# Performance work log

Measured on AMD Instinct MI355X. Metric: run time of the kernel, lower is better.

## Reference

```python
import jax, jax.numpy as jnp
import numpy as np

N_ITER = 4  # matches init_kwargs n_iter
N, K, D = 32768, 32, 32


def setup_inputs() -> dict:
    key = jax.random.key(0)
    k1, k2 = jax.random.split(key)
    data = jax.random.normal(k1, (N, D), dtype=jnp.float32)
    # torch init: means ~ randn, covariances = stacked identity, weights uniform
    means = jax.random.normal(k2, (K, D), dtype=jnp.float32)
    covariances = jnp.tile(jnp.eye(D, dtype=jnp.float32)[None], (K, 1, 1))
    weights = jnp.ones((K,), dtype=jnp.float32) / K
    return {"data": data, "means": means, "covariances": covariances, "weights": weights}


def _em(data, means, covariances, weights, n_iter):
    for _ in range(n_iter):
        # ---- E-step (vectorized over components, replacing the python loop) ----
        inv = jnp.linalg.inv(covariances)          # [K,D,D]
        det = jnp.linalg.det(covariances)          # [K]
        diff = data[:, None, :] - means[None]      # [N,K,D]
        # quadratic form diff^T Sigma^{-1} diff per point/component
        q = jnp.einsum('nkd,kde,nke->nk', diff, inv, diff)  # [N,K]
        probs = weights[None, :] * jnp.exp(-0.5 * q) / jnp.sqrt(det)[None, :]
        probs = probs / probs.sum(axis=1, keepdims=True)    # responsibilities [N,K]
        # ---- M-step (torch updates weights first; cov uses diff w.r.t. OLD means) ----
        weights = probs.mean(axis=0)                         # [K]
        Nk = probs.sum(axis=0)                               # [K]
        means = (probs.T @ data) / Nk[:, None]               # [K,D] (new means)
        covariances = jnp.einsum('nk,nkd,nke->kde', probs, diff, diff) / Nk[:, None, None]
    return means, covariances, weights


def reference(data, means, covariances, weights):
    return _em(data, means, covariances, weights, N_ITER)
```

## Files before the change

### kernel.cpp

```cpp
#include <hip/hip_runtime.h>

#define NPTS 32768
#define KK 32
#define DD 32

__global__ __launch_bounds__(256) void init_kernel(
    const float* __restrict__ means0, const float* __restrict__ cov0,
    const float* __restrict__ w0,
    float* __restrict__ meansA, float* __restrict__ covS, float* __restrict__ wS)
{
    int i = blockIdx.x * 256 + threadIdx.x;
    if (i < 1024)  meansA[i] = means0[i];
    if (i < 32768) covS[i]   = cov0[i];
    if (i < 32)    wS[i]     = w0[i];
}

__global__ __launch_bounds__(256) void prep_kernel(
    const float* __restrict__ cov, const float* __restrict__ means_in,
    const float* __restrict__ wts,
    float* __restrict__ A2, float* __restrict__ b2,
    float* __restrict__ cvec, float* __restrict__ coef)
{
    int k   = blockIdx.x;
    int tid = threadIdx.x;
    __shared__ float M[32][66];
    __shared__ float mu[32];
    __shared__ float bb[32];

    for (int i = tid; i < 1024; i += 256) {
        int r = i >> 5, c = i & 31;
        M[r][c]      = cov[k * 1024 + i];
        M[r][32 + c] = (r == c) ? 1.0f : 0.0f;
    }
    if (tid < 32) mu[tid] = means_in[k * 32 + tid];
    __syncthreads();

    int r  = tid >> 3;
    int c0 = (tid & 7) * 8;
    float det = 1.0f;
    for (int s = 0; s < 32; ++s) {
        float piv = M[s][s];
        det *= piv;
        float rp = 1.0f / piv;
        float f  = (r != s) ? M[r][s] : 0.0f;
        __syncthreads();
        if (tid < 64) M[s][tid] *= rp;
        __syncthreads();
        if (r != s) {
            #pragma unroll
            for (int j = 0; j < 8; ++j) M[r][c0 + j] -= f * M[s][c0 + j];
        }
        __syncthreads();
    }

    for (int i = tid; i < 1024; i += 256) {
        int d = i >> 5, e = i & 31;
        float val = M[d][32 + e];
        A2[(i >> 1) * 64 + k * 2 + (i & 1)] = val;
    }
    if (tid < 32) {
        int d = tid;
        float bd = 0.0f;
        #pragma unroll
        for (int e = 0; e < 32; ++e) bd += M[d][32 + e] * mu[e];
        bb[d] = bd;
        b2[(d >> 1) * 64 + k * 2 + (d & 1)] = bd;
    }
    __syncthreads();
    if (tid == 0) {
        float cc = 0.0f;
        #pragma unroll
        for (int d = 0; d < 32; ++d) cc += mu[d] * bb[d];
        cvec[k] = cc;
        coef[k] = wts[k] / sqrtf(det);
    }
}

__global__ __launch_bounds__(1024) void estep_kernel(
    const float* __restrict__ data, const float* __restrict__ A2g,
    const float* __restrict__ b2g, const float* __restrict__ cvec,
    const float* __restrict__ coefg, float* __restrict__ P)
{
    __shared__ alignas(16) float A2s[32768];
    int tid = threadIdx.x;
    for (int i = tid; i < 8192; i += 1024)
        ((float4*)A2s)[i] = ((const float4*)A2g)[i];
    __syncthreads();

    int lane = tid & 63;
    int wv   = tid >> 6;
    int k    = lane & 31;
    int g    = lane >> 5;
    int p0   = blockIdx.x * 64 + wv * 4 + g * 2;

    float x0[32], x1[32];
    const float4* d0p = (const float4*)(data + (size_t)p0 * 32);
    const float4* d1p = (const float4*)(data + (size_t)(p0 + 1) * 32);
    #pragma unroll
    for (int j = 0; j < 8; ++j) {
        float4 v = d0p[j];
        x0[4*j] = v.x; x0[4*j+1] = v.y; x0[4*j+2] = v.z; x0[4*j+3] = v.w;
        float4 u = d1p[j];
        x1[4*j] = u.x; x1[4*j+1] = u.y; x1[4*j+2] = u.z; x1[4*j+3] = u.w;
    }

    float q0 = 0.0f, q1 = 0.0f;
    #pragma unroll
    for (int d = 0; d < 32; ++d) {
        float r0 = 0.0f, s0 = 0.0f, r1 = 0.0f, s1 = 0.0f;
        #pragma unroll
        for (int c = 0; c < 16; ++c) {
            float2 a = *(const float2*)&A2s[(d * 16 + c) * 64 + (k << 1)];
            r0 += a.x * x0[2*c];     s0 += a.y * x0[2*c + 1];
            r1 += a.x * x1[2*c];     s1 += a.y * x1[2*c + 1];
        }
        q0 += x0[d] * (r0 + s0);
        q1 += x1[d] * (r1 + s1);
    }

    float bx0 = 0.0f, bx1 = 0.0f;
    #pragma unroll
    for (int d2 = 0; d2 < 16; ++d2) {
        float2 b = *(const float2*)&b2g[d2 * 64 + (k << 1)];
        bx0 += b.x * x0[2*d2] + b.y * x0[2*d2 + 1];
        bx1 += b.x * x1[2*d2] + b.y * x1[2*d2 + 1];
    }
    float cc = cvec[k], cf = coefg[k];
    float e0 = cf * __expf(-0.5f * (q0 - 2.0f * bx0 + cc));
    float e1 = cf * __expf(-0.5f * (q1 - 2.0f * bx1 + cc));

    float s0r = e0, s1r = e1;
    #pragma unroll
    for (int m = 16; m >= 1; m >>= 1) {
        s0r += __shfl_xor(s0r, m, 64);
        s1r += __shfl_xor(s1r, m, 64);
    }
    P[(size_t)p0 * 32 + k]       = e0 / s0r;
    P[(size_t)(p0 + 1) * 32 + k] = e1 / s1r;
}

#define PSTRIDE 1060
__global__ __launch_bounds__(256) void mstep_kernel(
    const float* __restrict__ data, const float* __restrict__ P,
    float* __restrict__ partial)
{
    int k     = blockIdx.x & 31;
    int chunk = blockIdx.x >> 5;
    int tid   = threadIdx.x;
    int g     = tid >> 7;
    int t     = tid & 127;
    int dp    = t >> 3;
    int eq    = t & 7;

    __shared__ alignas(16) float Xf[128 * 32];
    __shared__ float Sc[128 * 11];

    float S00=0,S01=0,S02=0,S03=0,S10=0,S11=0,S12=0,S13=0;
    float m0 = 0.0f, m1 = 0.0f, nk = 0.0f;
    int base = chunk * 1024;

    for (int tile = 0; tile < 8; ++tile) {
        __syncthreads();
        for (int i = tid; i < 1024; i += 256)
            ((float4*)Xf)[i] = ((const float4*)(data + (size_t)(base + tile * 128) * 32))[i];
        __syncthreads();
        int n0 = g * 64;
        for (int n = 0; n < 64; ++n) {
            int gn  = base + tile * 128 + n0 + n;
            float p = P[(size_t)gn * 32 + k];
            float2 xd = *(const float2*)&Xf[(n0 + n) * 32 + 2 * dp];
            float4 xe = *(const float4*)&Xf[(n0 + n) * 32 + 4 * eq];
            float px0 = p * xd.x, px1 = p * xd.y;
            S00 += px0 * xe.x; S01 += px0 * xe.y; S02 += px0 * xe.z; S03 += px0 * xe.w;
            S10 += px1 * xe.x; S11 += px1 * xe.y; S12 += px1 * xe.z; S13 += px1 * xe.w;
            m0 += px0; m1 += px1;
            nk += p;
        }
    }
    __syncthreads();
    if (g == 1) {
        Sc[t*11+0]=S00; Sc[t*11+1]=S01; Sc[t*11+2]=S02; Sc[t*11+3]=S03;
        Sc[t*11+4]=S10; Sc[t*11+5]=S11; Sc[t*11+6]=S12; Sc[t*11+7]=S13;
        Sc[t*11+8]=m0;  Sc[t*11+9]=m1;  Sc[t*11+10]=nk;
    }
    __syncthreads();
    if (g == 0) {
        S00+=Sc[t*11+0]; S01+=Sc[t*11+1]; S02+=Sc[t*11+2]; S03+=Sc[t*11+3];
        S10+=Sc[t*11+4]; S11+=Sc[t*11+5]; S12+=Sc[t*11+6]; S13+=Sc[t*11+7];
        m0 +=Sc[t*11+8]; m1 +=Sc[t*11+9]; nk+=Sc[t*11+10];
        float* out = partial + (size_t)(chunk * 32 + k) * PSTRIDE;
        int d0 = 2 * dp, e0 = 4 * eq;
        out[d0*32 + e0 + 0] = S00; out[d0*32 + e0 + 1] = S01;
        out[d0*32 + e0 + 2] = S02; out[d0*32 + e0 + 3] = S03;
        out[(d0+1)*32 + e0 + 0] = S10; out[(d0+1)*32 + e0 + 1] = S11;
        out[(d0+1)*32 + e0 + 2] = S12; out[(d0+1)*32 + e0 + 3] = S13;
        if (eq == 0) { out[1024 + d0] = m0; out[1024 + d0 + 1] = m1; }
        if (t == 0)  out[1056] = nk;
    }
}

__global__ void reduce_mnk_kernel(const float* __restrict__ partial,
    float* __restrict__ Nk, float* __restrict__ mvec,
    float* __restrict__ means_out, float* __restrict__ weights_out)
{
    int k = blockIdx.x, tid = threadIdx.x;
    __shared__ float nksh;
    if (tid == 0) {
        float s = 0.0f;
        for (int ch = 0; ch < 32; ++ch) s += partial[(size_t)(ch * 32 + k) * PSTRIDE + 1056];
        Nk[k] = s; weights_out[k] = s / (float)NPTS; nksh = s;
    }
    __syncthreads();
    if (tid < 32) {
        float s = 0.0f;
        for (int ch = 0; ch < 32; ++ch) s += partial[(size_t)(ch * 32 + k) * PSTRIDE + 1024 + tid];
        mvec[k * 32 + tid] = s;
        means_out[k * 32 + tid] = s / nksh;
    }
}

__global__ __launch_bounds__(256) void cov_kernel(const float* __restrict__ partial,
    const float* __restrict__ Nk, const float* __restrict__ mvec,
    const float* __restrict__ means_old, float* __restrict__ cov_state)
{
    int idx = blockIdx.x * 256 + threadIdx.x;
    int k = idx >> 10, de = idx & 1023, d = de >> 5, e = de & 31;
    float s = 0.0f;
    for (int ch = 0; ch < 32; ++ch) s += partial[(size_t)(ch * 32 + k) * PSTRIDE + de];
    float nk   = Nk[k];
    float mu_d = means_old[k * 32 + d], mu_e = means_old[k * 32 + e];
    float mn_d = mvec[k * 32 + d] / nk, mn_e = mvec[k * 32 + e] / nk;
    cov_state[idx] = s / nk - mu_d * mn_e - mn_d * mu_e + mu_d * mu_e;
}

__global__ __launch_bounds__(256) void writeout_kernel(
    const float* __restrict__ means, const float* __restrict__ cov,
    const float* __restrict__ w, float* __restrict__ out)
{
    int i = blockIdx.x * 256 + threadIdx.x;
    if (i < 1024)  out[i] = means[i];
    if (i < 32768) out[1024 + i] = cov[i];
    if (i < 32)    out[33792 + i] = w[i];
}

extern "C" void kernel_launch(void* const* d_in, const int* in_sizes, int n_in,
                              void* d_out, int out_size, void* d_ws, size_t ws_size,
                              hipStream_t stream) {
    (void)in_sizes; (void)n_in; (void)out_size; (void)ws_size;
    const float* data   = (const float*)d_in[0];
    const float* means0 = (const float*)d_in[1];
    const float* cov0   = (const float*)d_in[2];
    const float* w0     = (const float*)d_in[3];

    float* ws      = (float*)d_ws;
    float* A2      = ws + 0;
    float* b2      = ws + 32768;
    float* cvec    = ws + 33792;
    float* coef    = ws + 33824;
    float* meansA  = ws + 33856;
    float* meansB  = ws + 34880;
    float* covS    = ws + 35904;
    float* wS      = ws + 68672;
    float* Nk      = ws + 68704;
    float* mvec    = ws + 68736;
    float* P       = ws + 69760;
    float* partial = ws + 1118336;

    init_kernel<<<128, 256, 0, stream>>>(means0, cov0, w0, meansA, covS, wS);
    float* mi = meansA;
    float* mo = meansB;
    for (int it = 0; it < 4; ++it) {
        prep_kernel<<<32, 256, 0, stream>>>(covS, mi, wS, A2, b2, cvec, coef);
        estep_kernel<<<512, 1024, 0, stream>>>(data, A2, b2, cvec, coef, P);
        mstep_kernel<<<1024, 256, 0, stream>>>(data, P, partial);
        reduce_mnk_kernel<<<32, 64, 0, stream>>>(partial, Nk, mvec, mo, wS);
        cov_kernel<<<128, 256, 0, stream>>>(partial, Nk, mvec, mi, covS);
        float* tmp = mi; mi = mo; mo = tmp;
    }
    writeout_kernel<<<128, 256, 0, stream>>>(mi, covS, wS, (float*)d_out);
}
```

Baseline: 568.4 us.

## Fuse EM finalize kernels, retile M-step accumulation, and widen E-step per-thread work

```diff
diff --git a/kernel.cpp b/kernel.cpp
--- a/kernel.cpp
+++ b/kernel.cpp
@@ -1,19 +1,7 @@
 #include <hip/hip_runtime.h>
 
 #define NPTS 32768
-#define KK 32
-#define DD 32
-
-__global__ __launch_bounds__(256) void init_kernel(
-    const float* __restrict__ means0, const float* __restrict__ cov0,
-    const float* __restrict__ w0,
-    float* __restrict__ meansA, float* __restrict__ covS, float* __restrict__ wS)
-{
-    int i = blockIdx.x * 256 + threadIdx.x;
-    if (i < 1024)  meansA[i] = means0[i];
-    if (i < 32768) covS[i]   = cov0[i];
-    if (i < 32)    wS[i]     = w0[i];
-}
+#define PREC 1057
 
 __global__ __launch_bounds__(256) void prep_kernel(
     const float* __restrict__ cov, const float* __restrict__ means_in,
@@ -55,8 +43,7 @@
 
     for (int i = tid; i < 1024; i += 256) {
         int d = i >> 5, e = i & 31;
-        float val = M[d][32 + e];
-        A2[(i >> 1) * 64 + k * 2 + (i & 1)] = val;
+        A2[(i >> 1) * 64 + k * 2 + (i & 1)] = M[d][32 + e];
     }
     if (tid < 32) {
         int d = tid;
@@ -76,14 +63,14 @@
     }
 }
 
-__global__ __launch_bounds__(1024) void estep_kernel(
+__global__ __launch_bounds__(512, 2) void estep_kernel(
     const float* __restrict__ data, const float* __restrict__ A2g,
     const float* __restrict__ b2g, const float* __restrict__ cvec,
     const float* __restrict__ coefg, float* __restrict__ P)
 {
     __shared__ alignas(16) float A2s[32768];
     int tid = threadIdx.x;
-    for (int i = tid; i < 8192; i += 1024)
+    for (int i = tid; i < 8192; i += 512)
         ((float4*)A2s)[i] = ((const float4*)A2g)[i];
     __syncthreads();
 
@@ -91,156 +78,194 @@
     int wv   = tid >> 6;
     int k    = lane & 31;
     int g    = lane >> 5;
-    int p0   = blockIdx.x * 64 + wv * 4 + g * 2;
-
-    float x0[32], x1[32];
-    const float4* d0p = (const float4*)(data + (size_t)p0 * 32);
-    const float4* d1p = (const float4*)(data + (size_t)(p0 + 1) * 32);
-    #pragma unroll
-    for (int j = 0; j < 8; ++j) {
-        float4 v = d0p[j];
-        x0[4*j] = v.x; x0[4*j+1] = v.y; x0[4*j+2] = v.z; x0[4*j+3] = v.w;
-        float4 u = d1p[j];
-        x1[4*j] = u.x; x1[4*j+1] = u.y; x1[4*j+2] = u.z; x1[4*j+3] = u.w;
-    }
-
-    float q0 = 0.0f, q1 = 0.0f;
+    int p0   = blockIdx.x * 64 + wv * 8 + g * 4;
+
+    float x0[32], x1[32], x2[32], x3[32];
+    {
+        const float4* dp0 = (const float4*)(data + (size_t)p0 * 32);
+        const float4* dp1 = (const float4*)(data + (size_t)(p0 + 1) * 32);
+        const float4* dp2 = (const float4*)(data + (size_t)(p0 + 2) * 32);
+        const float4* dp3 = (const float4*)(data + (size_t)(p0 + 3) * 32);
+        #pragma unroll
+        for (int j = 0; j < 8; ++j) {
+            float4 v0 = dp0[j]; x0[4*j]=v0.x; x0[4*j+1]=v0.y; x0[4*j+2]=v0.z; x0[4*j+3]=v0.w;
+            float4 v1 = dp1[j]; x1[4*j]=v1.x; x1[4*j+1]=v1.y; x1[4*j+2]=v1.z; x1[4*j+3]=v1.w;
+            float4 v2 = dp2[j]; x2[4*j]=v2.x; x2[4*j+1]=v2.y; x2[4*j+2]=v2.z; x2[4*j+3]=v2.w;
+            float4 v3 = dp3[j]; x3[4*j]=v3.x; x3[4*j+1]=v3.y; x3[4*j+2]=v3.z; x3[4*j+3]=v3.w;
+        }
+    }
+
+    float q0 = 0.0f, q1 = 0.0f, q2 = 0.0f, q3 = 0.0f;
     #pragma unroll
     for (int d = 0; d < 32; ++d) {
-        float r0 = 0.0f, s0 = 0.0f, r1 = 0.0f, s1 = 0.0f;
+        float r0=0, s0=0, r1=0, s1=0, r2=0, s2=0, r3=0, s3=0;
         #pragma unroll
         for (int c = 0; c < 16; ++c) {
             float2 a = *(const float2*)&A2s[(d * 16 + c) * 64 + (k << 1)];
-            r0 += a.x * x0[2*c];     s0 += a.y * x0[2*c + 1];
-            r1 += a.x * x1[2*c];     s1 += a.y * x1[2*c + 1];
+            r0 += a.x * x0[2*c];  s0 += a.y * x0[2*c+1];
+            r1 += a.x * x1[2*c];  s1 += a.y * x1[2*c+1];
+            r2 += a.x * x2[2*c];  s2 += a.y * x2[2*c+1];
+            r3 += a.x * x3[2*c];  s3 += a.y * x3[2*c+1];
         }
         q0 += x0[d] * (r0 + s0);
         q1 += x1[d] * (r1 + s1);
-    }
-
-    float bx0 = 0.0f, bx1 = 0.0f;
+        q2 += x2[d] * (r2 + s2);
+        q3 += x3[d] * (r3 + s3);
+    }
+
+    float b0=0, b1=0, b2v=0, b3=0;
     #pragma unroll
     for (int d2 = 0; d2 < 16; ++d2) {
         float2 b = *(const float2*)&b2g[d2 * 64 + (k << 1)];
-        bx0 += b.x * x0[2*d2] + b.y * x0[2*d2 + 1];
-        bx1 += b.x * x1[2*d2] + b.y * x1[2*d2 + 1];
+        b0 += b.x * x0[2*d2] + b.y * x0[2*d2+1];
+        b1 += b.x * x1[2*d2] + b.y * x1[2*d2+1];
+        b2v+= b.x * x2[2*d2] + b.y * x2[2*d2+1];
+        b3 += b.x * x3[2*d2] + b.y * x3[2*d2+1];
     }
     float cc = cvec[k], cf = coefg[k];
-    float e0 = cf * __expf(-0.5f * (q0 - 2.0f * bx0 + cc));
-    float e1 = cf * __expf(-0.5f * (q1 - 2.0f * bx1 + cc));
-
-    float s0r = e0, s1r = e1;
+    float e0 = cf * __expf(-0.5f * (q0 - 2.0f * b0  + cc));
+    float e1 = cf * __expf(-0.5f * (q1 - 2.0f * b1  + cc));
+    float e2 = cf * __expf(-0.5f * (q2 - 2.0f * b2v + cc));
+    float e3 = cf * __expf(-0.5f * (q3 - 2.0f * b3  + cc));
+
+    float t0=e0, t1=e1, t2=e2, t3=e3;
     #pragma unroll
     for (int m = 16; m >= 1; m >>= 1) {
-        s0r += __shfl_xor(s0r, m, 64);
-        s1r += __shfl_xor(s1r, m, 64);
-    }
-    P[(size_t)p0 * 32 + k]       = e0 / s0r;
-    P[(size_t)(p0 + 1) * 32 + k] = e1 / s1r;
-}
-
-#define PSTRIDE 1060
-__global__ __launch_bounds__(256) void mstep_kernel(
+        t0 += __shfl_xor(t0, m, 64);
+        t1 += __shfl_xor(t1, m, 64);
+        t2 += __shfl_xor(t2, m, 64);
+        t3 += __shfl_xor(t3, m, 64);
+    }
+    P[(size_t)p0 * 32 + k]       = e0 / t0;
+    P[(size_t)(p0 + 1) * 32 + k] = e1 / t1;
+    P[(size_t)(p0 + 2) * 32 + k] = e2 / t2;
+    P[(size_t)(p0 + 3) * 32 + k] = e3 / t3;
+}
+
+__global__ __launch_bounds__(256, 4) void mstep_kernel(
     const float* __restrict__ data, const float* __restrict__ P,
     float* __restrict__ partial)
 {
     int k     = blockIdx.x & 31;
     int chunk = blockIdx.x >> 5;
     int tid   = threadIdx.x;
-    int g     = tid >> 7;
-    int t     = tid & 127;
-    int dp    = t >> 3;
-    int eq    = t & 7;
-
-    __shared__ alignas(16) float Xf[128 * 32];
-    __shared__ float Sc[128 * 11];
-
-    float S00=0,S01=0,S02=0,S03=0,S10=0,S11=0,S12=0,S13=0;
-    float m0 = 0.0f, m1 = 0.0f, nk = 0.0f;
+    int tile  = tid & 31;
+    int ng    = tid >> 5;
+    int dt    = tile >> 2;
+    int et    = tile & 3;
+
+    __shared__ alignas(16) float SH[8 * 1088];
+
+    float acc[4][8];
+    #pragma unroll
+    for (int i = 0; i < 4; ++i)
+        #pragma unroll
+        for (int j = 0; j < 8; ++j) acc[i][j] = 0.0f;
+    float m0=0, m1=0, m2=0, m3=0, nk=0;
+
     int base = chunk * 1024;
-
-    for (int tile = 0; tile < 8; ++tile) {
-        __syncthreads();
-        for (int i = tid; i < 1024; i += 256)
-            ((float4*)Xf)[i] = ((const float4*)(data + (size_t)(base + tile * 128) * 32))[i];
-        __syncthreads();
-        int n0 = g * 64;
-        for (int n = 0; n < 64; ++n) {
-            int gn  = base + tile * 128 + n0 + n;
-            float p = P[(size_t)gn * 32 + k];
-            float2 xd = *(const float2*)&Xf[(n0 + n) * 32 + 2 * dp];
-            float4 xe = *(const float4*)&Xf[(n0 + n) * 32 + 4 * eq];
-            float px0 = p * xd.x, px1 = p * xd.y;
-            S00 += px0 * xe.x; S01 += px0 * xe.y; S02 += px0 * xe.z; S03 += px0 * xe.w;
-            S10 += px1 * xe.x; S11 += px1 * xe.y; S12 += px1 * xe.z; S13 += px1 * xe.w;
-            m0 += px0; m1 += px1;
-            nk += p;
-        }
-    }
-    __syncthreads();
-    if (g == 1) {
-        Sc[t*11+0]=S00; Sc[t*11+1]=S01; Sc[t*11+2]=S02; Sc[t*11+3]=S03;
-        Sc[t*11+4]=S10; Sc[t*11+5]=S11; Sc[t*11+6]=S12; Sc[t*11+7]=S13;
-        Sc[t*11+8]=m0;  Sc[t*11+9]=m1;  Sc[t*11+10]=nk;
-    }
-    __syncthreads();
-    if (g == 0) {
-        S00+=Sc[t*11+0]; S01+=Sc[t*11+1]; S02+=Sc[t*11+2]; S03+=Sc[t*11+3];
-        S10+=Sc[t*11+4]; S11+=Sc[t*11+5]; S12+=Sc[t*11+6]; S13+=Sc[t*11+7];
-        m0 +=Sc[t*11+8]; m1 +=Sc[t*11+9]; nk+=Sc[t*11+10];
-        float* out = partial + (size_t)(chunk * 32 + k) * PSTRIDE;
-        int d0 = 2 * dp, e0 = 4 * eq;
-        out[d0*32 + e0 + 0] = S00; out[d0*32 + e0 + 1] = S01;
-        out[d0*32 + e0 + 2] = S02; out[d0*32 + e0 + 3] = S03;
-        out[(d0+1)*32 + e0 + 0] = S10; out[(d0+1)*32 + e0 + 1] = S11;
-        out[(d0+1)*32 + e0 + 2] = S12; out[(d0+1)*32 + e0 + 3] = S13;
-        if (eq == 0) { out[1024 + d0] = m0; out[1024 + d0 + 1] = m1; }
-        if (t == 0)  out[1056] = nk;
-    }
-}
-
-__global__ void reduce_mnk_kernel(const float* __restrict__ partial,
-    float* __restrict__ Nk, float* __restrict__ mvec,
-    float* __restrict__ means_out, float* __restrict__ weights_out)
+    for (int stage = 0; stage < 4; ++stage) {
+        __syncthreads();
+        for (int i = tid; i < 2048; i += 256)
+            ((float4*)SH)[i] = ((const float4*)(data + (size_t)(base + stage * 256) * 32))[i];
+        __syncthreads();
+        const float4* X4 = (const float4*)SH;
+        int nb = ng * 32;
+        #pragma unroll 4
+        for (int nn = 0; nn < 32; ++nn) {
+            int n  = nb + nn;
+            float p = P[(size_t)(base + stage * 256 + n) * 32 + k];
+            float4 xd  = X4[n * 8 + dt];
+            float4 xe0 = X4[n * 8 + et * 2];
+            float4 xe1 = X4[n * 8 + et * 2 + 1];
+            float p0 = p * xd.x, p1 = p * xd.y, p2 = p * xd.z, p3 = p * xd.w;
+            acc[0][0]+=p0*xe0.x; acc[0][1]+=p0*xe0.y; acc[0][2]+=p0*xe0.z; acc[0][3]+=p0*xe0.w;
+            acc[0][4]+=p0*xe1.x; acc[0][5]+=p0*xe1.y; acc[0][6]+=p0*xe1.z; acc[0][7]+=p0*xe1.w;
+            acc[1][0]+=p1*xe0.x; acc[1][1]+=p1*xe0.y; acc[1][2]+=p1*xe0.z; acc[1][3]+=p1*xe0.w;
+            acc[1][4]+=p1*xe1.x; acc[1][5]+=p1*xe1.y; acc[1][6]+=p1*xe1.z; acc[1][7]+=p1*xe1.w;
+            acc[2][0]+=p2*xe0.x; acc[2][1]+=p2*xe0.y; acc[2][2]+=p2*xe0.z; acc[2][3]+=p2*xe0.w;
+            acc[2][4]+=p2*xe1.x; acc[2][5]+=p2*xe1.y; acc[2][6]+=p2*xe1.z; acc[2][7]+=p2*xe1.w;
+            acc[3][0]+=p3*xe0.x; acc[3][1]+=p3*xe0.y; acc[3][2]+=p3*xe0.z; acc[3][3]+=p3*xe0.w;
+            acc[3][4]+=p3*xe1.x; acc[3][5]+=p3*xe1.y; acc[3][6]+=p3*xe1.z; acc[3][7]+=p3*xe1.w;
+            if (et == 0) { m0 += p0; m1 += p1; m2 += p2; m3 += p3; }
+            if (tile == 0) nk += p;
+        }
+    }
+    __syncthreads();
+
+    {
+        float* Sg = SH + ng * 1088;
+        #pragma unroll
+        for (int i = 0; i < 4; ++i) {
+            int row = dt * 4 + i;
+            #pragma unroll
+            for (int j = 0; j < 8; ++j) {
+                int col = (et * 8 + j + dt) & 31;
+                Sg[row * 32 + col] = acc[i][j];
+            }
+        }
+        if (et == 0) {
+            Sg[1024 + dt * 4 + 0] = m0; Sg[1024 + dt * 4 + 1] = m1;
+            Sg[1024 + dt * 4 + 2] = m2; Sg[1024 + dt * 4 + 3] = m3;
+        }
+        if (tile == 0) Sg[1056] = nk;
+    }
+    __syncthreads();
+
+    float* out = partial + (size_t)(chunk * 32 + k) * PREC;
+    for (int e = tid; e < PREC; e += 256) {
+        int ridx;
+        if (e < 1024) {
+            int row = e >> 5, col = e & 31;
+            ridx = row * 32 + ((col + (row >> 2)) & 31);
+        } else ridx = e;
+        float s = 0.0f;
+        #pragma unroll
+        for (int gg = 0; gg < 8; ++gg) s += SH[gg * 1088 + ridx];
+        out[e] = s;
+    }
+}
+
+__global__ __launch_bounds__(256) void finalize_kernel(
+    const float* __restrict__ partial, const float* __restrict__ means_old,
+    float* __restrict__ covS, float* __restrict__ means_new_ws,
+    float* __restrict__ wS, float* __restrict__ out)
 {
     int k = blockIdx.x, tid = threadIdx.x;
-    __shared__ float nksh;
+    __shared__ float SS[PREC];
+    __shared__ float MU[32];
+    __shared__ float MB[32];
+
+    for (int e = tid; e < PREC; e += 256) {
+        float s = 0.0f;
+        for (int ch = 0; ch < 32; ++ch)
+            s += partial[(size_t)(ch * 32 + k) * PREC + e];
+        SS[e] = s;
+    }
+    if (tid < 32) MU[tid] = means_old[k * 32 + tid];
+    __syncthreads();
+
+    float nk = SS[1056];
+    float rnk = 1.0f / nk;
+    if (tid < 32) {
+        float mb = SS[1024 + tid] * rnk;
+        MB[tid] = mb;
+        means_new_ws[k * 32 + tid] = mb;
+        out[k * 32 + tid] = mb;
+    }
+    __syncthreads();
+
+    for (int idx = tid; idx < 1024; idx += 256) {
+        int d = idx >> 5, e = idx & 31;
+        float c = SS[idx] * rnk - MU[d] * MB[e] - MB[d] * MU[e] + MU[d] * MU[e];
+        covS[k * 1024 + idx] = c;
+        out[1024 + k * 1024 + idx] = c;
+    }
     if (tid == 0) {
-        float s = 0.0f;
-        for (int ch = 0; ch < 32; ++ch) s += partial[(size_t)(ch * 32 + k) * PSTRIDE + 1056];
-        Nk[k] = s; weights_out[k] = s / (float)NPTS; nksh = s;
-    }
-    __syncthreads();
-    if (tid < 32) {
-        float s = 0.0f;
-        for (int ch = 0; ch < 32; ++ch) s += partial[(size_t)(ch * 32 + k) * PSTRIDE + 1024 + tid];
-        mvec[k * 32 + tid] = s;
-        means_out[k * 32 + tid] = s / nksh;
-    }
-}
-
-__global__ __launch_bounds__(256) void cov_kernel(const float* __restrict__ partial,
-    const float* __restrict__ Nk, const float* __restrict__ mvec,
-    const float* __restrict__ means_old, float* __restrict__ cov_state)
-{
-    int idx = blockIdx.x * 256 + threadIdx.x;
-    int k = idx >> 10, de = idx & 1023, d = de >> 5, e = de & 31;
-    float s = 0.0f;
-    for (int ch = 0; ch < 32; ++ch) s += partial[(size_t)(ch * 32 + k) * PSTRIDE + de];
-    float nk   = Nk[k];
-    float mu_d = means_old[k * 32 + d], mu_e = means_old[k * 32 + e];
-    float mn_d = mvec[k * 32 + d] / nk, mn_e = mvec[k * 32 + e] / nk;
-    cov_state[idx] = s / nk - mu_d * mn_e - mn_d * mu_e + mu_d * mu_e;
-}
-
-__global__ __launch_bounds__(256) void writeout_kernel(
-    const float* __restrict__ means, const float* __restrict__ cov,
-    const float* __restrict__ w, float* __restrict__ out)
-{
-    int i = blockIdx.x * 256 + threadIdx.x;
-    if (i < 1024)  out[i] = means[i];
-    if (i < 32768) out[1024 + i] = cov[i];
-    if (i < 32)    out[33792 + i] = w[i];
+        float w = nk * (1.0f / (float)NPTS);
+        wS[k] = w;
+        out[33792 + k] = w;
+    }
 }
 
 extern "C" void kernel_launch(void* const* d_in, const int* in_sizes, int n_in,
@@ -261,21 +286,19 @@
     float* meansB  = ws + 34880;
     float* covS    = ws + 35904;
     float* wS      = ws + 68672;
-    float* Nk      = ws + 68704;
-    float* mvec    = ws + 68736;
-    float* P       = ws + 69760;
-    float* partial = ws + 1118336;
-
-    init_kernel<<<128, 256, 0, stream>>>(means0, cov0, w0, meansA, covS, wS);
+    float* P       = ws + 68704;
+    float* partial = ws + 1117280;
+
     float* mi = meansA;
     float* mo = meansB;
     for (int it = 0; it < 4; ++it) {
-        prep_kernel<<<32, 256, 0, stream>>>(covS, mi, wS, A2, b2, cvec, coef);
-        estep_kernel<<<512, 1024, 0, stream>>>(data, A2, b2, cvec, coef, P);
+        const float* cov_src = (it == 0) ? cov0   : covS;
+        const float* mns_src = (it == 0) ? means0 : mi;
+        const float* w_src   = (it == 0) ? w0     : wS;
+        prep_kernel<<<32, 256, 0, stream>>>(cov_src, mns_src, w_src, A2, b2, cvec, coef);
+        estep_kernel<<<512, 512, 0, stream>>>(data, A2, b2, cvec, coef, P);
         mstep_kernel<<<1024, 256, 0, stream>>>(data, P, partial);
-        reduce_mnk_kernel<<<32, 64, 0, stream>>>(partial, Nk, mvec, mo, wS);
-        cov_kernel<<<128, 256, 0, stream>>>(partial, Nk, mvec, mi, covS);
+        finalize_kernel<<<32, 256, 0, stream>>>(partial, mns_src, covS, mo, wS, (float*)d_out);
         float* tmp = mi; mi = mo; mo = tmp;
     }
-    writeout_kernel<<<128, 256, 0, stream>>>(mi, covS, wS, (float*)d_out);
-}
+}
```

After: 500.1 us. 12.0% less time.
